# Optimization experiments

Hardware: AMD Instinct MI355X
Metric: run time of the kernel (lower is better)

The kernel has to match this reference:

```python
import jax, jax.numpy as jnp
import numpy as np


def _ln(x, g, b, eps=1e-5):
    mu = jnp.mean(x, axis=-1, keepdims=True)
    var = jnp.mean((x - mu) ** 2, axis=-1, keepdims=True)
    return (x - mu) * jax.lax.rsqrt(var + eps) * g + b


def setup_inputs() -> dict:
    key = jax.random.key(0)
    ks = jax.random.split(key, 12)
    B, H, W, D = 16, 128, 128, 64
    N = H * W
    Dff = 4 * D
    s = 0.02
    f32 = jnp.float32
    return {
        "x": jax.random.normal(ks[0], (B, N, D), f32),
        "H": H,
        "W": W,
        "ln1_scale": jnp.ones((D,), f32),
        "ln1_bias": jnp.zeros((D,), f32),
        "Wk": jax.random.normal(ks[1], (D, D), f32) * s,
        "bk": jnp.zeros((D,), f32),
        "Wq": jax.random.normal(ks[2], (D, D), f32) * s,
        "bq": jnp.zeros((D,), f32),
        "Wv": jax.random.normal(ks[3], (D, D), f32) * s,
        "bv": jnp.zeros((D,), f32),
        "Wr": jax.random.normal(ks[4], (D, D), f32) * s,
        "br": jnp.zeros((D,), f32),
        "ln2_scale": jnp.ones((D,), f32),
        "ln2_bias": jnp.zeros((D,), f32),
        "W1": jax.random.normal(ks[5], (Dff, D), f32) * s,
        "b1": jnp.zeros((Dff,), f32),
        "dw_w": jax.random.normal(ks[6], (Dff, 1, 3, 3), f32) * s,
        "dw_b": jnp.zeros((Dff,), f32),
        "W2": jax.random.normal(ks[7], (D, Dff), f32) * s,
        "b2": jnp.zeros((D,), f32),
    }


def reference(x, H, W, ln1_scale, ln1_bias, Wk, bk, Wq, bq, Wv, bv, Wr, br,
              ln2_scale, ln2_bias, W1, b1, dw_w, dw_b, W2, b2):
    B, N, D = x.shape
    Dff = W1.shape[0]

    # ---- EfficientAttention (head_count=1), tokens kept as [B, N, C] ----
    n1 = _ln(x, ln1_scale, ln1_bias)
    # 1x1 convs on [B,D,H,W] == per-token linear projections
    k = jax.nn.softmax(n1 @ Wk.T + bk, axis=1)    # softmax over spatial dim N (torch dim=2 of [B,Ck,N])
    q = jax.nn.softmax(n1 @ Wq.T + bq, axis=-1)   # softmax over key channels (torch dim=1)
    v = n1 @ Wv.T + bv                            # [B,N,Cv]
    context = jnp.einsum('bnk,bnv->bkv', k, v)    # key @ value^T, tiny [B,Ck,Cv]
    att = jnp.einsum('bkv,bnk->bnv', context, q)  # context^T @ query -> [B,N,Cv]
    attn_out = att @ Wr.T + br                    # reprojection 1x1 conv
    tx = x + attn_out

    # ---- MixFFN: fc1 -> depthwise 3x3 -> GELU -> fc2 ----
    n2 = _ln(tx, ln2_scale, ln2_bias)
    h = n2 @ W1.T + b1                            # [B,N,Dff]
    himg = jnp.transpose(h, (0, 2, 1)).reshape(B, Dff, H, W)
    conv = jax.lax.conv_general_dilated(
        himg, dw_w, window_strides=(1, 1), padding='SAME',
        feature_group_count=Dff,
        dimension_numbers=('NCHW', 'OIHW', 'NCHW')) + dw_b[None, :, None, None]
    h2 = jnp.transpose(conv.reshape(B, Dff, N), (0, 2, 1))
    h2 = jax.nn.gelu(h2, approximate=False)       # torch nn.GELU default is exact erf
    out = tx + (h2 @ W2.T + b2)
    return out
```

## Files before the change

### kernel.cpp

```cpp
#include <hip/hip_runtime.h>
#include <math.h>

typedef __bf16 bf16x8 __attribute__((ext_vector_type(8)));
typedef float f32x4 __attribute__((ext_vector_type(4)));
typedef unsigned short u16x8 __attribute__((ext_vector_type(8)));
typedef unsigned short u16x4v __attribute__((ext_vector_type(4)));

constexpr int NIMG = 16384;
constexpr int HPITCH = 130;
constexpr int HROW = HPITCH*256;

__device__ __forceinline__ unsigned short f2bf(float f){
  unsigned u = __builtin_bit_cast(unsigned, f);
  u += 0x7fffu + ((u>>16)&1u);
  return (unsigned short)(u>>16);
}
__device__ __forceinline__ unsigned pack2(float a, float b){
  return (unsigned)f2bf(a) | ((unsigned)f2bf(b)<<16);
}
__device__ __forceinline__ float bf2f(unsigned short h){
  unsigned u = ((unsigned)h)<<16;
  return __builtin_bit_cast(float, u);
}
__device__ __forceinline__ bf16x8 ldfrag_g(const unsigned short* p){
  u16x8 v = *reinterpret_cast<const u16x8*>(p);
  return __builtin_bit_cast(bf16x8, v);
}
__device__ __forceinline__ f32x4 mfma16(bf16x8 a, bf16x8 b, f32x4 c){
  return __builtin_amdgcn_mfma_f32_16x16x32_bf16(a, b, c, 0, 0, 0);
}
__device__ __forceinline__ float gelu_fast(float v){
  float u = v*v;
  float arg = v*(-1.5957691216057308f - 0.0713548162726009f*u);
  return v*__builtin_amdgcn_rcpf(1.f + __expf(arg));
}

__global__ __launch_bounds__(64) void k0_wfrag(
  const float* __restrict__ Wk, const float* __restrict__ Wq,
  const float* __restrict__ Wv, const float* __restrict__ Wr,
  const float* __restrict__ W1, const float* __restrict__ W2,
  const float* __restrict__ dww, float* __restrict__ dwp,
  unsigned short* __restrict__ wf)
{
  const int bid = blockIdx.x, l = threadIdx.x;
  if (bid == 96){
    #pragma unroll
    for (int c=0;c<4;++c){
      int f = l*4 + c;
      #pragma unroll
      for (int j=0;j<9;++j) dwp[f*12+j] = dww[f*9+j];
      dwp[f*12+9]=0.f; dwp[f*12+10]=0.f; dwp[f*12+11]=0.f;
    }
    return;
  }
  const float* src; int K, nt, ks; unsigned short* dst;
  if (bid < 32){
    int w = bid>>3, f = bid&7;
    src = (w==0)?Wk:(w==1)?Wq:(w==2)?Wv:Wr;
    K = 64; nt = f>>1; ks = f&1;
    dst = wf + w*4096 + f*512;
  } else if (bid < 64){
    int f = bid-32; src = W1; K = 64; nt = f>>1; ks = f&1;
    dst = wf + 16384 + f*512;
  } else {
    int f = bid-64; src = W2; K = 256; nt = f>>3; ks = f&7;
    dst = wf + 32768 + f*512;
  }
  u16x8 v;
  #pragma unroll
  for (int j=0;j<8;++j){
    int k = ks*32 + (l>>4)*8 + j;
    int n = nt*16 + (l&15);
    v[j] = f2bf(src[n*K + k]);
  }
  *reinterpret_cast<u16x8*>(dst + l*8) = v;
}

__global__ __launch_bounds__(256) void zhalo(unsigned* __restrict__ gh, unsigned* __restrict__ zr){
  int idx = blockIdx.x*256 + threadIdx.x;
  if (idx < 524288){
    int ch2 = idx & 127;
    int pos = idx >> 7;
    int side = pos & 1, row = pos >> 1;
    gh[(size_t)(row*HPITCH + side*(HPITCH-1))*128 + ch2] = 0;
  } else {
    int j = idx - 524288;
    if (j < HROW/2) zr[j] = 0;
  }
}

__global__ __launch_bounds__(256,2) void k1_ctx(
  const float* __restrict__ x, const float* __restrict__ g1, const float* __restrict__ be1,
  const float* __restrict__ bk, const float* __restrict__ bv,
  const unsigned short* __restrict__ wf,
  float* __restrict__ g_part, float* __restrict__ g_sump)
{
  __shared__ unsigned short tiles[4][4096];
  __shared__ float ctx_l[64*68];
  __shared__ float ssum_l[4][64];
  const int t = threadIdx.x, wid = t>>6, l = t&63;
  const int lg = l>>4, l15 = l&15;
  unsigned short* tile = tiles[wid];
  const int tok0 = blockIdx.x*512 + wid*128;

  bf16x8 WkF[8], WvF[8];
  #pragma unroll
  for (int f=0; f<8; ++f){
    WkF[f] = ldfrag_g(wf +    0 + f*512 + l*8);
    WvF[f] = ldfrag_g(wf + 8192 + f*512 + l*8);
  }
  float4 g1v  = *reinterpret_cast<const float4*>(&g1[l15*4]);
  float4 be1v = *reinterpret_cast<const float4*>(&be1[l15*4]);
  float bkv[4], bvv[4];
  #pragma unroll
  for (int ct=0; ct<4; ++ct){ bkv[ct]=bk[ct*16+l15]; bvv[ct]=bv[ct*16+l15]; }

  f32x4 acc[4][4];
  #pragma unroll
  for (int a=0;a<4;++a)
    #pragma unroll
    for (int b=0;b<4;++b) acc[a][b] = (f32x4){0.f,0.f,0.f,0.f};
  float sume[4] = {0.f,0.f,0.f,0.f};

  for (int tb=0; tb<2; ++tb){
    const int tbase = tok0 + tb*64;
    #pragma unroll
    for (int it=0; it<16; ++it){
      int row = it*4 + lg;
      float4 xv = *reinterpret_cast<const float4*>(&x[(size_t)(tbase+row)*64 + l15*4]);
      float s1 = xv.x+xv.y+xv.z+xv.w;
      float s2 = xv.x*xv.x + xv.y*xv.y + xv.z*xv.z + xv.w*xv.w;
      #pragma unroll
      for (int off=1; off<16; off<<=1){ s1 += __shfl_xor(s1,off,64); s2 += __shfl_xor(s2,off,64); }
      float mu = s1*(1.f/64.f);
      float rs = rsqrtf(s2*(1.f/64.f) - mu*mu + 1e-5f);
      uint2 pk = { pack2((xv.x-mu)*rs*g1v.x + be1v.x, (xv.y-mu)*rs*g1v.y + be1v.y),
                   pack2((xv.z-mu)*rs*g1v.z + be1v.z, (xv.w-mu)*rs*g1v.w + be1v.w) };
      *reinterpret_cast<uint2*>(&tile[row*64 + ((l15*4) ^ ((row&7)<<3))]) = pk;
    }
    bf16x8 aF[4][2];
    #pragma unroll
    for (int mt=0;mt<4;++mt){
      int row = mt*16+l15, sw=(row&7)<<3, ab=row*64;
      aF[mt][0] = __builtin_bit_cast(bf16x8, *reinterpret_cast<const u16x8*>(tile+ab+((     lg*8)^sw)));
      aF[mt][1] = __builtin_bit_cast(bf16x8, *reinterpret_cast<const u16x8*>(tile+ab+((32 + lg*8)^sw)));
    }
    #pragma unroll
    for (int half=0; half<2; ++half){
      #pragma unroll
      for (int m2=0;m2<2;++m2){
        const int mt = half*2+m2;
        #pragma unroll
        for (int ct=0;ct<4;++ct){
          f32x4 z = {0.f,0.f,0.f,0.f};
          z = mfma16(aF[mt][0], WkF[ct*2+0], z);
          z = mfma16(aF[mt][1], WkF[ct*2+1], z);
          float e0=__expf(z[0]+bkv[ct]), e1=__expf(z[1]+bkv[ct]);
          float e2=__expf(z[2]+bkv[ct]), e3=__expf(z[3]+bkv[ct]);
          sume[ct] += (e0+e1)+(e2+e3);
          const int c = ct*16+l15, sw = (c&7)<<3;
          const int cb = m2*16+lg*4;
          uint2 pe = { pack2(e0,e1), pack2(e2,e3) };
          *reinterpret_cast<uint2*>(&tile[c*64 + (cb ^ sw)]) = pe;
          f32x4 w = {0.f,0.f,0.f,0.f};
          w = mfma16(aF[mt][0], WvF[ct*2+0], w);
          w = mfma16(aF[mt][1], WvF[ct*2+1], w);
          uint2 pv = { pack2(w[0]+bvv[ct], w[1]+bvv[ct]), pack2(w[2]+bvv[ct], w[3]+bvv[ct]) };
          *reinterpret_cast<uint2*>(&tile[c*64 + ((32+cb) ^ sw)]) = pv;
        }
      }
      bf16x8 eA[4], vB[4];
      #pragma unroll
      for (int cm=0;cm<4;++cm){
        int row = cm*16+l15, sw=(row&7)<<3;
        eA[cm] = __builtin_bit_cast(bf16x8, *reinterpret_cast<const u16x8*>(tile + row*64 + ((     lg*8)^sw)));
        vB[cm] = __builtin_bit_cast(bf16x8, *reinterpret_cast<const u16x8*>(tile + row*64 + ((32 + lg*8)^sw)));
      }
      #pragma unroll
      for (int cm=0; cm<4; ++cm)
        #pragma unroll
        for (int jn=0; jn<4; ++jn)
          acc[cm][jn] = mfma16(eA[cm], vB[jn], acc[cm][jn]);
    }
  }
  #pragma unroll
  for (int ct=0; ct<4; ++ct){
    float s = sume[ct];
    s += __shfl_xor(s,16,64); s += __shfl_xor(s,32,64);
    if (lg==0) ssum_l[wid][ct*16+l15] = s;
  }
  #define CTX_RED(OP) \
    _Pragma("unroll") for (int cm=0;cm<4;++cm) \
    _Pragma("unroll") for (int jn=0;jn<4;++jn) \
    _Pragma("unroll") for (int r=0;r<4;++r) \
      ctx_l[(cm*16+lg*4+r)*68 + jn*16+l15] OP acc[cm][jn][r];
  if (wid==0){ CTX_RED(=) }  __syncthreads();
  if (wid==1){ CTX_RED(+=) } __syncthreads();
  if (wid==2){ CTX_RED(+=) } __syncthreads();
  if (wid==3){ CTX_RED(+=) } __syncthreads();
  #undef CTX_RED
  for (int i=t; i<4096; i+=256)
    g_part[(size_t)blockIdx.x*4096 + i] = ctx_l[(i>>6)*68 + (i&63)];
  if (t<64)
    g_sump[blockIdx.x*64 + t] = ssum_l[0][t]+ssum_l[1][t]+ssum_l[2][t]+ssum_l[3][t];
}

__global__ __launch_bounds__(512) void k15_ctxwr(
  const float* __restrict__ g_part, const float* __restrict__ g_sump,
  const float* __restrict__ Wr, unsigned short* __restrict__ ctxWrF)
{
  __shared__ float sctx[4096];
  __shared__ float sWr[4096];
  __shared__ float sinv[64];
  const int b = blockIdx.x, t = threadIdx.x;
  if (t<64){
    float s=0.f;
    #pragma unroll 8
    for (int p=0;p<32;++p) s += g_sump[(b*32+p)*64 + t];
    sinv[t] = 1.f/s;
  }
  for (int idx=t; idx<4096; idx+=512){
    float s=0.f;
    #pragma unroll 8
    for (int p=0;p<32;++p) s += g_part[(size_t)(b*32+p)*4096 + idx];
    sctx[idx] = s;
  }
  __syncthreads();
  {
    int c = t>>3, d0 = (t&7)*8;
    float invc = sinv[c];
    #pragma unroll
    for (int dd=0; dd<8; ++dd){
      int d = d0+dd; float s = 0.f;
      #pragma unroll
      for (int v=0; v<64; ++v) s += sctx[c*64+v]*Wr[d*64+v];
      sWr[c*64+d] = s*invc;
    }
  }
  __syncthreads();
  {
    int f = t>>6, l = t&63, nt = f>>1, ks = f&1;
    u16x8 v;
    #pragma unroll
    for (int j=0;j<8;++j){
      int k = ks*32 + (l>>4)*8 + j;
      int n = nt*16 + (l&15);
      v[j] = f2bf(sWr[k*64+n]);
    }
    *reinterpret_cast<u16x8*>(ctxWrF + b*4096 + f*512 + l*8) = v;
  }
}

__global__ __launch_bounds__(256,2) void k2_attn_ffn1(
  const float* __restrict__ x,
  const float* __restrict__ g1, const float* __restrict__ be1,
  const float* __restrict__ bq, const float* __restrict__ br,
  const float* __restrict__ g2, const float* __restrict__ be2,
  const float* __restrict__ b1,
  const unsigned short* __restrict__ wf,
  const unsigned short* __restrict__ ctxWrF,
  unsigned short* __restrict__ g_txb, unsigned short* __restrict__ g_h)
{
  __shared__ unsigned short tiles[4][4096];
  const int t = threadIdx.x, wid = t>>6, l = t&63;
  const int l15 = l&15, lg = l>>4;
  unsigned short* tile = tiles[wid];
  const int tok0 = (blockIdx.x*4 + wid)*64;
  const int img  = blockIdx.x>>6;
  const int yrow = (tok0>>7)&127;
  const int xb   = tok0&127;
  const size_t hbase = ((size_t)(img*128 + yrow)*HPITCH + 1 + xb)*256;

  bf16x8 WqF[8], CWF[8];
  #pragma unroll
  for (int f=0; f<8; ++f){
    WqF[f] = ldfrag_g(wf + 4096 + f*512 + l*8);
    CWF[f] = ldfrag_g(ctxWrF + img*4096 + f*512 + l*8);
  }
  float4 g1v  = *reinterpret_cast<const float4*>(&g1[l15*4]);
  float4 be1v = *reinterpret_cast<const float4*>(&be1[l15*4]);
  float bqv[4], brv[4], g2v[4], be2v[4];
  #pragma unroll
  for (int nt=0; nt<4; ++nt){
    bqv[nt]=bq[nt*16+l15]; brv[nt]=br[nt*16+l15];
    g2v[nt]=g2[nt*16+l15]; be2v[nt]=be2[nt*16+l15];
  }
  float b1v[16];
  #pragma unroll
  for (int i=0;i<16;++i) b1v[i]=b1[i*16+l15];

  #pragma unroll
  for (int it=0; it<16; ++it){
    int row = it*4 + lg;
    float4 xv = *reinterpret_cast<const float4*>(&x[(size_t)(tok0+row)*64 + l15*4]);
    float s1 = xv.x+xv.y+xv.z+xv.w;
    float s2 = xv.x*xv.x + xv.y*xv.y + xv.z*xv.z + xv.w*xv.w;
    #pragma unroll
    for (int off=1; off<16; off<<=1){ s1 += __shfl_xor(s1,off,64); s2 += __shfl_xor(s2,off,64); }
    float mu = s1*(1.f/64.f);
    float rs = rsqrtf(s2*(1.f/64.f) - mu*mu + 1e-5f);
    uint2 pk = { pack2((xv.x-mu)*rs*g1v.x + be1v.x, (xv.y-mu)*rs*g1v.y + be1v.y),
                 pack2((xv.z-mu)*rs*g1v.z + be1v.z, (xv.w-mu)*rs*g1v.w + be1v.w) };
    *reinterpret_cast<uint2*>(&tile[row*64 + ((l15*4) ^ ((row&7)<<3))]) = pk;
  }

  for (int mt=0; mt<4; ++mt){
    const int arow = mt*16 + l15;
    const int asw  = (arow&7)<<3;
    const int abase= arow*64;
    bf16x8 a0 = __builtin_bit_cast(bf16x8, *reinterpret_cast<const u16x8*>(tile + abase + ((     lg*8) ^ asw)));
    bf16x8 a1 = __builtin_bit_cast(bf16x8, *reinterpret_cast<const u16x8*>(tile + abase + ((32 + lg*8) ^ asw)));
    f32x4 qa[4];
    #pragma unroll
    for (int nt=0; nt<4; ++nt){
      f32x4 z = {0.f,0.f,0.f,0.f};
      z = mfma16(a0, WqF[nt*2+0], z);
      z = mfma16(a1, WqF[nt*2+1], z);
      qa[nt] = z;
    }
    #pragma unroll
    for (int nt=0; nt<4; ++nt)
      #pragma unroll
      for (int r=0; r<4; ++r) qa[nt][r] += bqv[nt];
    float mx[4];
    #pragma unroll
    for (int r=0;r<4;++r) mx[r] = fmaxf(fmaxf(qa[0][r],qa[1][r]), fmaxf(qa[2][r],qa[3][r]));
    #pragma unroll
    for (int off=1; off<16; off<<=1)
      #pragma unroll
      for (int r=0;r<4;++r) mx[r] = fmaxf(mx[r], __shfl_xor(mx[r], off, 64));
    float sm[4] = {0.f,0.f,0.f,0.f};
    #pragma unroll
    for (int nt=0;nt<4;++nt)
      #pragma unroll
      for (int r=0;r<4;++r){ float e = __expf(qa[nt][r]-mx[r]); qa[nt][r]=e; sm[r]+=e; }
    #pragma unroll
    for (int off=1; off<16; off<<=1)
      #pragma unroll
      for (int r=0;r<4;++r) sm[r] += __shfl_xor(sm[r], off, 64);
    float inv[4];
    #pragma unroll
    for (int r=0;r<4;++r) inv[r] = 1.f/sm[r];
    #pragma unroll
    for (int nt=0;nt<4;++nt)
      #pragma unroll
      for (int r=0;r<4;++r){
        int row = mt*16 + lg*4 + r, col = nt*16 + l15;
        tile[row*64 + (col ^ ((row&7)<<3))] = f2bf(qa[nt][r]*inv[r]);
      }
    bf16x8 p0 = __builtin_bit_cast(bf16x8, *reinterpret_cast<const u16x8*>(tile + abase + ((     lg*8) ^ asw)));
    bf16x8 p1 = __builtin_bit_cast(bf16x8, *reinterpret_cast<const u16x8*>(tile + abase + ((32 + lg*8) ^ asw)));
    f32x4 ao[4];
    #pragma unroll
    for (int nt=0; nt<4; ++nt){
      f32x4 z = {0.f,0.f,0.f,0.f};
      z = mfma16(p0, CWF[nt*2+0], z);
      z = mfma16(p1, CWF[nt*2+1], z);
      ao[nt] = z;
    }
    float txv[4][4];
    float s1v[4] = {0.f,0.f,0.f,0.f}, s2v[4] = {0.f,0.f,0.f,0.f};
    #pragma unroll
    for (int nt=0;nt<4;++nt)
      #pragma unroll
      for (int r=0;r<4;++r){
        size_t row = (size_t)(tok0 + mt*16 + lg*4 + r);
        float v = ao[nt][r] + brv[nt] + x[row*64 + nt*16+l15];
        g_txb[row*64 + nt*16+l15] = f2bf(v);
        txv[nt][r] = v; s1v[r] += v; s2v[r] += v*v;
      }
    #pragma unroll
    for (int off=1; off<16; off<<=1)
      #pragma unroll
      for (int r=0;r<4;++r){ s1v[r] += __shfl_xor(s1v[r], off, 64); s2v[r] += __shfl_xor(s2v[r], off, 64); }
    #pragma unroll
    for (int r=0;r<4;++r){
      float mu2 = s1v[r]*(1.f/64.f);
      float rs  = rsqrtf(s2v[r]*(1.f/64.f) - mu2*mu2 + 1e-5f);
      s1v[r] = mu2; s2v[r] = rs;
    }
    #pragma unroll
    for (int nt=0;nt<4;++nt)
      #pragma unroll
      for (int r=0;r<4;++r){
        int row = mt*16 + lg*4 + r, col = nt*16 + l15;
        float n2 = (txv[nt][r]-s1v[r])*s2v[r]*g2v[nt] + be2v[nt];
        tile[row*64 + (col ^ ((row&7)<<3))] = f2bf(n2);
      }
  }

  #pragma unroll 2
  for (int nt2=0; nt2<16; ++nt2){
    bf16x8 w0 = ldfrag_g(wf + 16384 + (nt2*2+0)*512 + l*8);
    bf16x8 w1 = ldfrag_g(wf + 16384 + (nt2*2+1)*512 + l*8);
    float bb = b1v[nt2];
    #pragma unroll
    for (int mt=0; mt<4; ++mt){
      const int arow = mt*16 + l15;
      const int asw  = (arow&7)<<3;
      const int abase= arow*64;
      bf16x8 n20 = __builtin_bit_cast(bf16x8, *reinterpret_cast<const u16x8*>(tile + abase + ((     lg*8) ^ asw)));
      bf16x8 n21 = __builtin_bit_cast(bf16x8, *reinterpret_cast<const u16x8*>(tile + abase + ((32 + lg*8) ^ asw)));
      f32x4 h = {bb,bb,bb,bb};
      h = mfma16(n20, w0, h);
      h = mfma16(n21, w1, h);
      #pragma unroll
      for (int r=0;r<4;++r)
        g_h[hbase + (size_t)(mt*16+lg*4+r)*256 + nt2*16 + l15] = f2bf(h[r]);
    }
  }
}

__global__ __launch_bounds__(256,2) void k3_conv_ffn2(
  const unsigned short* __restrict__ g_h,
  const unsigned short* __restrict__ zrow,
  const float* __restrict__ dwp, const float* __restrict__ dwb,
  const float* __restrict__ b2,
  const unsigned short* __restrict__ wf,
  const unsigned short* __restrict__ g_txb, float* __restrict__ out)
{
  __shared__ unsigned short tiles[4][4096];
  const int t = threadIdx.x, wid = t>>6, l = t&63;
  const int l15 = l&15, lg = l>>4;
  unsigned short* tile = tiles[wid];
  const int blk = (blockIdx.x & 7)*128 + (blockIdx.x >> 3);
  const int strip = blk*4 + wid;
  const int tok0 = strip*64;
  const int img  = tok0>>14;
  const int y    = (tok0>>7)&127;
  const int x0   = tok0&127;
  const bool okm = (y>0), okp = (y<127);
  const int p    = lg;
  const int ch   = l15;

  f32x4 oacc[4][4];
  #pragma unroll
  for (int a=0;a<4;++a)
    #pragma unroll
    for (int b=0;b<4;++b) oacc[a][b] = (f32x4){0.f,0.f,0.f,0.f};

  const size_t base = ((size_t)(img*128+y)*HPITCH + x0 + p*16)*256;

  for (int i=0;i<4;++i){
    const int f0 = i*64 + ch*4;
    float cw0[9], cw1[9], cw2[9], cw3[9];
    {
      float4 a0=*reinterpret_cast<const float4*>(&dwp[(f0+0)*12]);
      float4 a1=*reinterpret_cast<const float4*>(&dwp[(f0+0)*12+4]);
      float  a2=dwp[(f0+0)*12+8];
      cw0[0]=a0.x;cw0[1]=a0.y;cw0[2]=a0.z;cw0[3]=a0.w;cw0[4]=a1.x;cw0[5]=a1.y;cw0[6]=a1.z;cw0[7]=a1.w;cw0[8]=a2;
      float4 b0=*reinterpret_cast<const float4*>(&dwp[(f0+1)*12]);
      float4 b1v=*reinterpret_cast<const float4*>(&dwp[(f0+1)*12+4]);
      float  b2v_=dwp[(f0+1)*12+8];
      cw1[0]=b0.x;cw1[1]=b0.y;cw1[2]=b0.z;cw1[3]=b0.w;cw1[4]=b1v.x;cw1[5]=b1v.y;cw1[6]=b1v.z;cw1[7]=b1v.w;cw1[8]=b2v_;
      float4 c0=*reinterpret_cast<const float4*>(&dwp[(f0+2)*12]);
      float4 c1=*reinterpret_cast<const float4*>(&dwp[(f0+2)*12+4]);
      float  c2=dwp[(f0+2)*12+8];
      cw2[0]=c0.x;cw2[1]=c0.y;cw2[2]=c0.z;cw2[3]=c0.w;cw2[4]=c1.x;cw2[5]=c1.y;cw2[6]=c1.z;cw2[7]=c1.w;cw2[8]=c2;
      float4 d0=*reinterpret_cast<const float4*>(&dwp[(f0+3)*12]);
      float4 d1=*reinterpret_cast<const float4*>(&dwp[(f0+3)*12+4]);
      float  d2=dwp[(f0+3)*12+8];
      cw3[0]=d0.x;cw3[1]=d0.y;cw3[2]=d0.z;cw3[3]=d0.w;cw3[4]=d1.x;cw3[5]=d1.y;cw3[6]=d1.z;cw3[7]=d1.w;cw3[8]=d2;
    }
    float4 cbv = *reinterpret_cast<const float4*>(&dwb[f0]);
    const unsigned short* rB = g_h + base + f0;
    const unsigned short* rA = okm ? (rB - HROW) : (zrow + f0);
    const unsigned short* rC = okp ? (rB + HROW) : (zrow + f0);

    auto ld4 = [](const unsigned short* pp) -> float4 {
      u16x4v a = *reinterpret_cast<const u16x4v*>(pp);
      return make_float4(bf2f(a[0]), bf2f(a[1]), bf2f(a[2]), bf2f(a[3]));
    };
    float4 pA=ld4(rA), pB=ld4(rB), pC=ld4(rC);
    float4 cA=ld4(rA+256), cB=ld4(rB+256), cC=ld4(rC+256);
    #pragma unroll 4
    for (int s=0; s<16; ++s){
      float4 nA=ld4(rA+(s+2)*256), nB=ld4(rB+(s+2)*256), nC=ld4(rC+(s+2)*256);
      float4 a;
      a.x = cbv.x + cw0[0]*pA.x + cw0[1]*cA.x + cw0[2]*nA.x
                  + cw0[3]*pB.x + cw0[4]*cB.x + cw0[5]*nB.x
                  + cw0[6]*pC.x + cw0[7]*cC.x + cw0[8]*nC.x;
      a.y = cbv.y + cw1[0]*pA.y + cw1[1]*cA.y + cw1[2]*nA.y
                  + cw1[3]*pB.y + cw1[4]*cB.y + cw1[5]*nB.y
                  + cw1[6]*pC.y + cw1[7]*cC.y + cw1[8]*nC.y;
      a.z = cbv.z + cw2[0]*pA.z + cw2[1]*cA.z + cw2[2]*nA.z
                  + cw2[3]*pB.z + cw2[4]*cB.z + cw2[5]*nB.z
                  + cw2[6]*pC.z + cw2[7]*cC.z + cw2[8]*nC.z;
      a.w = cbv.w + cw3[0]*pA.w + cw3[1]*cA.w + cw3[2]*nA.w
                  + cw3[3]*pB.w + cw3[4]*cB.w + cw3[5]*nB.w
                  + cw3[6]*pC.w + cw3[7]*cC.w + cw3[8]*nC.w;
      int row = p*16 + s;
      uint2 pk = { pack2(gelu_fast(a.x), gelu_fast(a.y)),
                   pack2(gelu_fast(a.z), gelu_fast(a.w)) };
      *reinterpret_cast<uint2*>(&tile[row*64 + ((ch*4) ^ ((row&7)<<3))]) = pk;
      pA=cA; pB=cB; pC=cC; cA=nA; cB=nB; cC=nC;
    }
    bf16x8 W2F[8];
    #pragma unroll
    for (int q=0;q<8;++q){
      int ntc = q>>1, cks = q&1;
      W2F[q] = ldfrag_g(wf + 32768 + (ntc*8 + i*2 + cks)*512 + l*8);
    }
    #pragma unroll
    for (int mtk=0; mtk<4; ++mtk){
      int row = mtk*16 + l15;
      int sw = (row&7)<<3;
      bf16x8 fb0 = __builtin_bit_cast(bf16x8, *reinterpret_cast<const u16x8*>(tile + row*64 + ((     lg*8) ^ sw)));
      bf16x8 fb1 = __builtin_bit_cast(bf16x8, *reinterpret_cast<const u16x8*>(tile + row*64 + ((32 + lg*8) ^ sw)));
      #pragma unroll
      for (int ntc=0;ntc<4;++ntc){
        oacc[ntc][mtk] = mfma16(W2F[ntc*2+0], fb0, oacc[ntc][mtk]);
        oacc[ntc][mtk] = mfma16(W2F[ntc*2+1], fb1, oacc[ntc][mtk]);
      }
    }
  }
  #pragma unroll
  for (int mtk=0;mtk<4;++mtk){
    const size_t rowoff = (size_t)(tok0 + mtk*16 + l15)*64;
    #pragma unroll
    for (int ntc=0;ntc<4;++ntc){
      float4 b2q = *reinterpret_cast<const float4*>(&b2[ntc*16 + lg*4]);
      u16x4v tq = *reinterpret_cast<const u16x4v*>(&g_txb[rowoff + ntc*16 + lg*4]);
      float4 o;
      o.x = oacc[ntc][mtk][0] + b2q.x + bf2f(tq[0]);
      o.y = oacc[ntc][mtk][1] + b2q.y + bf2f(tq[1]);
      o.z = oacc[ntc][mtk][2] + b2q.z + bf2f(tq[2]);
      o.w = oacc[ntc][mtk][3] + b2q.w + bf2f(tq[3]);
      *reinterpret_cast<float4*>(&out[rowoff + ntc*16 + lg*4]) = o;
    }
  }
}

extern "C" void kernel_launch(void* const* d_in, const int* in_sizes, int n_in,
                              void* d_out, int out_size, void* d_ws, size_t ws_size,
                              hipStream_t stream)
{
  const float* x  =(const float*)d_in[0];
  const float* g1 =(const float*)d_in[3];
  const float* be1=(const float*)d_in[4];
  const float* Wk =(const float*)d_in[5];
  const float* bk =(const float*)d_in[6];
  const float* Wq =(const float*)d_in[7];
  const float* bq =(const float*)d_in[8];
  const float* Wv =(const float*)d_in[9];
  const float* bv =(const float*)d_in[10];
  const float* Wr =(const float*)d_in[11];
  const float* br =(const float*)d_in[12];
  const float* g2 =(const float*)d_in[13];
  const float* be2=(const float*)d_in[14];
  const float* W1 =(const float*)d_in[15];
  const float* b1 =(const float*)d_in[16];
  const float* dww=(const float*)d_in[17];
  const float* dwb=(const float*)d_in[18];
  const float* W2 =(const float*)d_in[19];
  const float* b2 =(const float*)d_in[20];
  float* outp = (float*)d_out;
  char* ws = (char*)d_ws;

  unsigned short* wfb    = (unsigned short*)ws;
  unsigned short* ctxWrF = (unsigned short*)(ws + 98304);
  float* g_sump = (float*)(ws + 229376);
  float* g_part = (float*)(ws + 393216);
  unsigned short* g_txb = (unsigned short*)(ws + 16777216);
  unsigned short* g_h   = (unsigned short*)(ws + 50331648);
  unsigned short* zr    = (unsigned short*)(ws + 186646528);
  float* dwp            = (float*)(ws + 186712064);

  hipLaunchKernelGGL(k0_wfrag, dim3(97), dim3(64), 0, stream, Wk, Wq, Wv, Wr, W1, W2, dww, dwp, wfb);
  hipLaunchKernelGGL(zhalo, dim3(2113), dim3(256), 0, stream, (unsigned*)g_h, (unsigned*)zr);
  hipLaunchKernelGGL(k1_ctx, dim3(512), dim3(256), 0, stream, x, g1, be1, bk, bv, wfb, g_part, g_sump);
  hipLaunchKernelGGL(k15_ctxwr, dim3(16), dim3(512), 0, stream, g_part, g_sump, Wr, ctxWrF);
  hipLaunchKernelGGL(k2_attn_ffn1, dim3(1024), dim3(256), 0, stream,
                     x, g1, be1, bq, br, g2, be2, b1, wfb, ctxWrF, g_txb, g_h);
  hipLaunchKernelGGL(k3_conv_ffn2, dim3(1024), dim3(256), 0, stream,
                     g_h, zr, dwp, dwb, b2, wfb, g_txb, outp);
}
```

Before: 253.8 us.

## Deepen dwconv load prefetch, vectorize weights, use exp2 GELU and hardware bf16 pack

The depthwise conv stage in the fc2 kernel now fully unrolls the 16-step column loop and issues raw bf16 loads six rows ahead, so more global loads are in flight. Conv weights are repacked channel-interleaved (index j*4+c) so each tap loads as one float4. The GELU approximation folds log2(e) into its constants to call exp2 directly, and the float-to-bf16 conversion uses the hardware v_cvt_pk_bf16_f32 instruction instead of manual rounding. The price is much higher register pressure from the 18-deep buffers, which may lower occupancy or cause spills.

```diff
diff --git a/kernel.cpp b/kernel.cpp
--- a/kernel.cpp
+++ b/kernel.cpp
@@ -29,10 +29,13 @@
 __device__ __forceinline__ f32x4 mfma16(bf16x8 a, bf16x8 b, f32x4 c){
   return __builtin_amdgcn_mfma_f32_16x16x32_bf16(a, b, c, 0, 0, 0);
 }
-__device__ __forceinline__ float gelu_fast(float v){
-  float u = v*v;
-  float arg = v*(-1.5957691216057308f - 0.0713548162726009f*u);
-  return v*__builtin_amdgcn_rcpf(1.f + __expf(arg));
+__device__ __forceinline__ f32x4 bfcvt4(uint2 q){
+  f32x4 r;
+  r[0] = __builtin_bit_cast(float, q.x << 16);
+  r[1] = __builtin_bit_cast(float, q.x & 0xffff0000u);
+  r[2] = __builtin_bit_cast(float, q.y << 16);
+  r[3] = __builtin_bit_cast(float, q.y & 0xffff0000u);
+  return r;
 }
 
 __global__ __launch_bounds__(64) void k0_wfrag(
@@ -48,8 +51,7 @@
     for (int c=0;c<4;++c){
       int f = l*4 + c;
       #pragma unroll
-      for (int j=0;j<9;++j) dwp[f*12+j] = dww[f*9+j];
-      dwp[f*12+9]=0.f; dwp[f*12+10]=0.f; dwp[f*12+11]=0.f;
+      for (int j=0;j<9;++j) dwp[l*36 + j*4 + c] = dww[f*9+j];
     }
     return;
   }
@@ -441,59 +443,62 @@
 
   const size_t base = ((size_t)(img*128+y)*HPITCH + x0 + p*16)*256;
 
+  const f32x4 kC0 = {-2.3022082f,-2.3022082f,-2.3022082f,-2.3022082f};
+  const f32x4 kC1 = {-0.1029432f,-0.1029432f,-0.1029432f,-0.1029432f};
+  const f32x4 kOne = {1.f,1.f,1.f,1.f};
+
   for (int i=0;i<4;++i){
     const int f0 = i*64 + ch*4;
-    float cw0[9], cw1[9], cw2[9], cw3[9];
-    {
-      float4 a0=*reinterpret_cast<const float4*>(&dwp[(f0+0)*12]);
-      float4 a1=*reinterpret_cast<const float4*>(&dwp[(f0+0)*12+4]);
-      float  a2=dwp[(f0+0)*12+8];
-      cw0[0]=a0.x;cw0[1]=a0.y;cw0[2]=a0.z;cw0[3]=a0.w;cw0[4]=a1.x;cw0[5]=a1.y;cw0[6]=a1.z;cw0[7]=a1.w;cw0[8]=a2;
-      float4 b0=*reinterpret_cast<const float4*>(&dwp[(f0+1)*12]);
-      float4 b1v=*reinterpret_cast<const float4*>(&dwp[(f0+1)*12+4]);
-      float  b2v_=dwp[(f0+1)*12+8];
-      cw1[0]=b0.x;cw1[1]=b0.y;cw1[2]=b0.z;cw1[3]=b0.w;cw1[4]=b1v.x;cw1[5]=b1v.y;cw1[6]=b1v.z;cw1[7]=b1v.w;cw1[8]=b2v_;
-      float4 c0=*reinterpret_cast<const float4*>(&dwp[(f0+2)*12]);
-      float4 c1=*reinterpret_cast<const float4*>(&dwp[(f0+2)*12+4]);
-      float  c2=dwp[(f0+2)*12+8];
-      cw2[0]=c0.x;cw2[1]=c0.y;cw2[2]=c0.z;cw2[3]=c0.w;cw2[4]=c1.x;cw2[5]=c1.y;cw2[6]=c1.z;cw2[7]=c1.w;cw2[8]=c2;
-      float4 d0=*reinterpret_cast<const float4*>(&dwp[(f0+3)*12]);
-      float4 d1=*reinterpret_cast<const float4*>(&dwp[(f0+3)*12+4]);
-      float  d2=dwp[(f0+3)*12+8];
-      cw3[0]=d0.x;cw3[1]=d0.y;cw3[2]=d0.z;cw3[3]=d0.w;cw3[4]=d1.x;cw3[5]=d1.y;cw3[6]=d1.z;cw3[7]=d1.w;cw3[8]=d2;
-    }
-    float4 cbv = *reinterpret_cast<const float4*>(&dwb[f0]);
+    f32x4 cw4[9];
+    #pragma unroll
+    for (int j=0;j<9;++j)
+      cw4[j] = *reinterpret_cast<const f32x4*>(&dwp[(i*16+ch)*36 + j*4]);
+    float4 cb4 = *reinterpret_cast<const float4*>(&dwb[f0]);
+    f32x4 cbv = {cb4.x, cb4.y, cb4.z, cb4.w};
+
     const unsigned short* rB = g_h + base + f0;
     const unsigned short* rA = okm ? (rB - HROW) : (zrow + f0);
     const unsigned short* rC = okp ? (rB + HROW) : (zrow + f0);
 
-    auto ld4 = [](const unsigned short* pp) -> float4 {
-      u16x4v a = *reinterpret_cast<const u16x4v*>(pp);
-      return make_float4(bf2f(a[0]), bf2f(a[1]), bf2f(a[2]), bf2f(a[3]));
-    };
-    float4 pA=ld4(rA), pB=ld4(rB), pC=ld4(rC);
-    float4 cA=ld4(rA+256), cB=ld4(rB+256), cC=ld4(rC+256);
-    #pragma unroll 4
-    for (int s=0; s<16; ++s){
-      float4 nA=ld4(rA+(s+2)*256), nB=ld4(rB+(s+2)*256), nC=ld4(rC+(s+2)*256);
-      float4 a;
-      a.x = cbv.x + cw0[0]*pA.x + cw0[1]*cA.x + cw0[2]*nA.x
-                  + cw0[3]*pB.x + cw0[4]*cB.x + cw0[5]*nB.x
-                  + cw0[6]*pC.x + cw0[7]*cC.x + cw0[8]*nC.x;
-      a.y = cbv.y + cw1[0]*pA.y + cw1[1]*cA.y + cw1[2]*nA.y
-                  + cw1[3]*pB.y + cw1[4]*cB.y + cw1[5]*nB.y
-                  + cw1[6]*pC.y + cw1[7]*cC.y + cw1[8]*nC.y;
-      a.z = cbv.z + cw2[0]*pA.z + cw2[1]*cA.z + cw2[2]*nA.z
-                  + cw2[3]*pB.z + cw2[4]*cB.z + cw2[5]*nB.z
-                  + cw2[6]*pC.z + cw2[7]*cC.z + cw2[8]*nC.z;
-      a.w = cbv.w + cw3[0]*pA.w + cw3[1]*cA.w + cw3[2]*nA.w
-                  + cw3[3]*pB.w + cw3[4]*cB.w + cw3[5]*nB.w
-                  + cw3[6]*pC.w + cw3[7]*cC.w + cw3[8]*nC.w;
+    uint2 qA[18], qB[18], qC[18];
+    f32x4 fA[18], fB[18], fC[18];
+    #pragma unroll
+    for (int o=0;o<6;++o){
+      qA[o] = *reinterpret_cast<const uint2*>(rA + o*256);
+      qB[o] = *reinterpret_cast<const uint2*>(rB + o*256);
+      qC[o] = *reinterpret_cast<const uint2*>(rC + o*256);
+    }
+    fA[0]=bfcvt4(qA[0]); fB[0]=bfcvt4(qB[0]); fC[0]=bfcvt4(qC[0]);
+    fA[1]=bfcvt4(qA[1]); fB[1]=bfcvt4(qB[1]); fC[1]=bfcvt4(qC[1]);
+    #pragma unroll
+    for (int s=0;s<16;++s){
+      if (s<12){
+        qA[s+6] = *reinterpret_cast<const uint2*>(rA + (s+6)*256);
+        qB[s+6] = *reinterpret_cast<const uint2*>(rB + (s+6)*256);
+        qC[s+6] = *reinterpret_cast<const uint2*>(rC + (s+6)*256);
+      }
+      fA[s+2]=bfcvt4(qA[s+2]); fB[s+2]=bfcvt4(qB[s+2]); fC[s+2]=bfcvt4(qC[s+2]);
+      f32x4 a = cbv;
+      a += cw4[0]*fA[s]; a += cw4[1]*fA[s+1]; a += cw4[2]*fA[s+2];
+      a += cw4[3]*fB[s]; a += cw4[4]*fB[s+1]; a += cw4[5]*fB[s+2];
+      a += cw4[6]*fC[s]; a += cw4[7]*fC[s+1]; a += cw4[8]*fC[s+2];
+      f32x4 u = a*a;
+      f32x4 w = u*kC1 + kC0;
+      f32x4 arg = a*w;
+      f32x4 e;
+      e[0]=__builtin_amdgcn_exp2f(arg[0]); e[1]=__builtin_amdgcn_exp2f(arg[1]);
+      e[2]=__builtin_amdgcn_exp2f(arg[2]); e[3]=__builtin_amdgcn_exp2f(arg[3]);
+      f32x4 den = e + kOne;
+      f32x4 rc;
+      rc[0]=__builtin_amdgcn_rcpf(den[0]); rc[1]=__builtin_amdgcn_rcpf(den[1]);
+      rc[2]=__builtin_amdgcn_rcpf(den[2]); rc[3]=__builtin_amdgcn_rcpf(den[3]);
+      f32x4 g = a*rc;
+      unsigned lo, hi;
+      asm("v_cvt_pk_bf16_f32 %0, %1, %2" : "=v"(lo) : "v"(g[0]), "v"(g[1]));
+      asm("v_cvt_pk_bf16_f32 %0, %1, %2" : "=v"(hi) : "v"(g[2]), "v"(g[3]));
+      uint2 pk = { lo, hi };
       int row = p*16 + s;
-      uint2 pk = { pack2(gelu_fast(a.x), gelu_fast(a.y)),
-                   pack2(gelu_fast(a.z), gelu_fast(a.w)) };
       *reinterpret_cast<uint2*>(&tile[row*64 + ((ch*4) ^ ((row&7)<<3))]) = pk;
-      pA=cA; pB=cB; pC=cC; cA=nA; cB=nB; cC=nC;
     }
     bf16x8 W2F[8];
     #pragma unroll
```

Result: slower. 263.5 us (+3.8%).
